# Optimization experiments

Hardware: AMD Instinct MI355X
Metric: run time of the kernel (lower is better)

## Reference

```python
import jax, jax.numpy as jnp
import numpy as np
import math

B, N, D = 4, 1024, 512
L, H, DH = 6, 8, 64
FF_INNER = 4 * D
NUM_BUCKETS, MAX_DIST = 32, 128
SCALE = 16.0  # cosine_sim_scale
ROT_DIM = 32  # min(32, dim_head)


def layernorm(x, g, stable=False, eps=1e-5):
    if stable:
        x = x / jax.lax.stop_gradient(jnp.max(x, axis=-1, keepdims=True))
    mean = jnp.mean(x, axis=-1, keepdims=True)
    var = jnp.mean(jnp.square(x - mean), axis=-1, keepdims=True)  # unbiased=False
    return (x - mean) * jax.lax.rsqrt(var + eps) * g


def l2norm(x, eps=1e-12):
    return x / jnp.maximum(jnp.linalg.norm(x, axis=-1, keepdims=True), eps)


def rotary_freqs(n):
    inv_freq = 1.0 / (10000.0 ** (jnp.arange(0, ROT_DIM, 2, dtype=jnp.float32) / ROT_DIM))
    f = jnp.arange(n, dtype=jnp.float32)[:, None] * inv_freq[None, :]  # [n, ROT_DIM/2]
    return jnp.repeat(f, 2, axis=-1)  # [n, ROT_DIM], interleaved pairs


def apply_rotary(t, freqs):
    # rotate only first ROT_DIM dims (rotary_embedding_torch semantics)
    rot, passd = t[..., :ROT_DIM], t[..., ROT_DIM:]
    x = rot.reshape(*rot.shape[:-1], ROT_DIM // 2, 2)
    rotated = jnp.stack((-x[..., 1], x[..., 0]), axis=-1).reshape(rot.shape)
    rot = rot * jnp.cos(freqs) + rotated * jnp.sin(freqs)
    return jnp.concatenate([rot, passd], axis=-1)


def rel_pos_bias(emb, i, j):
    # T5-style causal relative position buckets
    rel = jnp.arange(j)[None, :] - jnp.arange(i)[:, None]
    n = jnp.maximum(-rel, 0)
    max_exact = NUM_BUCKETS // 2
    val_large = max_exact + (
        jnp.log(jnp.maximum(n, 1).astype(jnp.float32) / max_exact)
        / math.log(MAX_DIST / max_exact) * (NUM_BUCKETS - max_exact)
    ).astype(jnp.int32)
    val_large = jnp.minimum(val_large, NUM_BUCKETS - 1)
    bucket = jnp.where(n < max_exact, n, val_large)
    return emb[bucket].transpose(2, 0, 1)  # [h, i, j]


def setup_inputs() -> dict:
    key = jax.random.key(0)
    ks = jax.random.split(key, 9)
    s = 0.02
    return {
        "x": jax.random.normal(ks[0], (B, N, D), jnp.float32),
        "rel_pos_emb": jax.random.normal(ks[1], (NUM_BUCKETS, H), jnp.float32) * s,
        "g_attn": jnp.ones((L, D), jnp.float32),
        "null_kv": jax.random.normal(ks[2], (L, 2, DH), jnp.float32),
        "Wq": jax.random.normal(ks[3], (L, D, H * DH), jnp.float32) * s,
        "Wkv": jax.random.normal(ks[4], (L, D, 2 * DH), jnp.float32) * s,
        "Wo": jax.random.normal(ks[5], (L, H * DH, D), jnp.float32) * s,
        "g_attn_out": jnp.ones((L, D), jnp.float32),
        "g_ff": jnp.ones((L, D), jnp.float32),
        "W1": jax.random.normal(ks[6], (L, D, 2 * FF_INNER), jnp.float32) * s,
        "W2": jax.random.normal(ks[7], (L, FF_INNER, D), jnp.float32) * s,
        "g_final": jnp.ones((D,), jnp.float32),
        "W_proj": jax.random.normal(ks[8], (D, D), jnp.float32) * s,
    }


def reference(x, rel_pos_emb, g_attn, null_kv, Wq, Wkv, Wo, g_attn_out, g_ff, W1, W2, g_final, W_proj):
    b, n, d = x.shape
    freqs = rotary_freqs(n)
    bias = rel_pos_bias(rel_pos_emb, n, n + 1)          # [h, n, n+1] (null kv column at j=0)
    causal = jnp.triu(jnp.ones((n, n + 1), dtype=bool), k=2)  # .triu(j - i + 1)
    neg = -jnp.finfo(x.dtype).max
    for l in range(L):
        # --- attention block ---
        xn = layernorm(x, g_attn[l])
        q = (xn @ Wq[l]).reshape(b, n, H, DH).transpose(0, 2, 1, 3) * SCALE  # b h n d
        k, v = jnp.split(xn @ Wkv[l], 2, axis=-1)                            # b n d (single-head kv)
        q = apply_rotary(q, freqs)
        k = apply_rotary(k, freqs)
        k = jnp.concatenate([jnp.broadcast_to(null_kv[l, 0], (b, 1, DH)), k], axis=1)
        v = jnp.concatenate([jnp.broadcast_to(null_kv[l, 1], (b, 1, DH)), v], axis=1)
        qn = l2norm(q) * math.sqrt(SCALE)   # cosine-sim attention
        kn = l2norm(k) * math.sqrt(SCALE)
        sim = jnp.einsum('bhid,bjd->bhij', qn, kn) + bias
        sim = jnp.where(causal, neg, sim)
        attn = jax.nn.softmax(sim.astype(jnp.float32), axis=-1).astype(x.dtype)
        o = jnp.einsum('bhij,bjd->bhid', attn, v).transpose(0, 2, 1, 3).reshape(b, n, H * DH)
        x = x + layernorm(o @ Wo[l], g_attn_out[l])
        # --- SwiGLU feedforward block ---
        hn = layernorm(x, g_ff[l])
        a, gate = jnp.split(hn @ W1[l], 2, axis=-1)
        x = x + (a * jax.nn.silu(gate)) @ W2[l]
    out = layernorm(x, g_final, stable=True)
    return out @ W_proj
```

## Files before the change

### kernel.cpp

```cpp
#include <hip/hip_runtime.h>
#include <hip/hip_bf16.h>
#include <cmath>

using bf16 = __hip_bfloat16;
typedef __bf16 v8bf __attribute__((ext_vector_type(8)));
typedef __bf16 v4bf __attribute__((ext_vector_type(4)));
typedef float  v4f  __attribute__((ext_vector_type(4)));

__device__ __forceinline__ float bf2f(bf16 x) { return __bfloat162float(x); }
__device__ __forceinline__ bf16  f2bf(float x) { return __float2bfloat16(x); }
__device__ __forceinline__ __bf16 tobf(float x) {
    bf16 h = __float2bfloat16(x);
    return __builtin_bit_cast(__bf16, h);
}

__device__ __forceinline__ void gll16(const bf16* g, bf16* l) {
    __builtin_amdgcn_global_load_lds(
        (const __attribute__((address_space(1))) unsigned int*)g,
        (__attribute__((address_space(3))) unsigned int*)l, 16, 0, 0);
}

__device__ __forceinline__ float ldin(const void* p, size_t i, int isf32) {
    if (isf32) return ((const float*)p)[i];
    return bf2f(((const bf16*)p)[i]);
}

__device__ __forceinline__ void ld8(const void* p, size_t base, int f, float v[8]) {
    if (f) {
        const float* pf = (const float*)p + base;
        float4 a = *(const float4*)pf, b = *(const float4*)(pf + 4);
        v[0]=a.x; v[1]=a.y; v[2]=a.z; v[3]=a.w;
        v[4]=b.x; v[5]=b.y; v[6]=b.z; v[7]=b.w;
    } else {
        v8bf a = *(const v8bf*)((const bf16*)p + base);
#pragma unroll
        for (int j = 0; j < 8; ++j) v[j] = (float)a[j];
    }
}

__device__ __forceinline__ float wave_sum(float v) {
#pragma unroll
    for (int o = 32; o > 0; o >>= 1) v += __shfl_xor(v, o, 64);
    return v;
}
__device__ __forceinline__ float wave_max(float v) {
#pragma unroll
    for (int o = 32; o > 0; o >>= 1) v = fmaxf(v, __shfl_xor(v, o, 64));
    return v;
}

__global__ void detect_k(const unsigned short* __restrict__ x, int* __restrict__ flag)
{
    __shared__ int s;
    int t = threadIdx.x;
    if (t == 0) s = 0;
    __syncthreads();
    int bad = 0;
    for (int i = t; i < 4096; i += 256) {
        int e = (x[i] >> 7) & 0xFF;
        if (e >= 147) bad++;
    }
    atomicAdd(&s, bad);
    __syncthreads();
    if (t == 0) *flag = (s > 64) ? 1 : 0;
}

__global__ __launch_bounds__(256)
void gemm_bt_silu(const bf16* __restrict__ A, const bf16* __restrict__ BT,
                  bf16* __restrict__ U, int K, int lda)
{
    __shared__ bf16 As[128 * 32];
    __shared__ bf16 Bs[128 * 32];
    const int t = threadIdx.x;
    const int lane = t & 63;
    const int wave = t >> 6;
    const int wm = (wave >> 1) * 64;
    const int wn = (wave & 1) * 64;
    const int bm = blockIdx.x * 128;
    const int bn = blockIdx.y * 128;
    const int fr = lane & 15;
    const int fk = (lane >> 4) * 8;

    v4f acc[4][4];
#pragma unroll
    for (int i = 0; i < 4; ++i)
#pragma unroll
        for (int j = 0; j < 4; ++j) { v4f z = {0.f, 0.f, 0.f, 0.f}; acc[i][j] = z; }

    for (int k0 = 0; k0 < K; k0 += 32) {
#pragma unroll
        for (int r = 0; r < 2; ++r) {
            int c = t + 256 * r;
            int row = c >> 2;
            int koff = (c & 3) * 8;
            gll16(A + (size_t)(bm + row) * lda + k0 + koff, &As[c * 8]);
            gll16(BT + (size_t)(bn + row) * K + k0 + koff, &Bs[c * 8]);
        }
        __syncthreads();
        v8bf af[4], bfr[4];
#pragma unroll
        for (int mt = 0; mt < 4; ++mt)
            af[mt] = *(const v8bf*)(&As[(wm + mt * 16 + fr) * 32 + fk]);
#pragma unroll
        for (int nt = 0; nt < 4; ++nt)
            bfr[nt] = *(const v8bf*)(&Bs[(wn + nt * 16 + fr) * 32 + fk]);
#pragma unroll
        for (int mt = 0; mt < 4; ++mt)
#pragma unroll
            for (int nt = 0; nt < 4; ++nt)
                acc[mt][nt] = __builtin_amdgcn_mfma_f32_16x16x32_bf16(
                    af[mt], bfr[nt], acc[mt][nt], 0, 0, 0);
        __syncthreads();
    }
    const int r0 = (lane >> 4) * 4;
    const int gbase = ((bn + wn) >> 6) * 32;
#pragma unroll
    for (int mt = 0; mt < 4; ++mt)
#pragma unroll
        for (int nt = 0; nt < 2; ++nt)
#pragma unroll
            for (int r = 0; r < 4; ++r) {
                int row = bm + wm + mt * 16 + r0 + r;
                int col = gbase + nt * 16 + fr;
                float a  = acc[mt][nt][r];
                float gg = acc[mt][nt + 2][r];
                U[(size_t)row * 2048 + col] = f2bf(a * (gg / (1.f + __expf(-gg))));
            }
}

__global__ __launch_bounds__(256)
void gemm64(const bf16* __restrict__ A, const bf16* __restrict__ BT,
            bf16* __restrict__ C, int M, int N, int K, int lda)
{
    __shared__ bf16 As[64 * 32];
    __shared__ bf16 Bs[128 * 32];
    const int t = threadIdx.x;
    const int lane = t & 63;
    const int wave = t >> 6;
    const int wm = (wave >> 1) * 32;
    const int wn = (wave & 1) * 64;
    const int bm = blockIdx.x * 64;
    const int bn = blockIdx.y * 128;
    const int fr = lane & 15;
    const int fk = (lane >> 4) * 8;

    v4f acc[2][4];
#pragma unroll
    for (int i = 0; i < 2; ++i)
#pragma unroll
        for (int j = 0; j < 4; ++j) { v4f z = {0.f, 0.f, 0.f, 0.f}; acc[i][j] = z; }

    for (int k0 = 0; k0 < K; k0 += 32) {
        {
            int row = t >> 2, koff = (t & 3) * 8;
            gll16(A + (size_t)(bm + row) * lda + k0 + koff, &As[t * 8]);
        }
#pragma unroll
        for (int r = 0; r < 2; ++r) {
            int c = t + 256 * r;
            int row = c >> 2, koff = (c & 3) * 8;
            gll16(BT + (size_t)(bn + row) * K + k0 + koff, &Bs[c * 8]);
        }
        __syncthreads();
        v8bf af[2], bfr[4];
#pragma unroll
        for (int mt = 0; mt < 2; ++mt)
            af[mt] = *(const v8bf*)(&As[(wm + mt * 16 + fr) * 32 + fk]);
#pragma unroll
        for (int nt = 0; nt < 4; ++nt)
            bfr[nt] = *(const v8bf*)(&Bs[(wn + nt * 16 + fr) * 32 + fk]);
#pragma unroll
        for (int mt = 0; mt < 2; ++mt)
#pragma unroll
            for (int nt = 0; nt < 4; ++nt)
                acc[mt][nt] = __builtin_amdgcn_mfma_f32_16x16x32_bf16(
                    af[mt], bfr[nt], acc[mt][nt], 0, 0, 0);
        __syncthreads();
    }
    const int r0 = (lane >> 4) * 4;
#pragma unroll
    for (int mt = 0; mt < 2; ++mt)
#pragma unroll
        for (int nt = 0; nt < 4; ++nt)
#pragma unroll
            for (int r = 0; r < 4; ++r) {
                int row = bm + wm + mt * 16 + r0 + r;
                int col = bn + wn + nt * 16 + fr;
                C[(size_t)row * N + col] = f2bf(acc[mt][nt][r]);
            }
}

__global__ __launch_bounds__(256)
void gemm64_out(const bf16* __restrict__ A, const bf16* __restrict__ BT,
                void* __restrict__ C, int M, int N, int K, int lda,
                const int* __restrict__ flag)
{
    __shared__ bf16 As[64 * 32];
    __shared__ bf16 Bs[128 * 32];
    const int f = *flag;
    const int t = threadIdx.x;
    const int lane = t & 63;
    const int wave = t >> 6;
    const int wm = (wave >> 1) * 32;
    const int wn = (wave & 1) * 64;
    const int bm = blockIdx.x * 64;
    const int bn = blockIdx.y * 128;
    const int fr = lane & 15;
    const int fk = (lane >> 4) * 8;

    v4f acc[2][4];
#pragma unroll
    for (int i = 0; i < 2; ++i)
#pragma unroll
        for (int j = 0; j < 4; ++j) { v4f z = {0.f, 0.f, 0.f, 0.f}; acc[i][j] = z; }

    for (int k0 = 0; k0 < K; k0 += 32) {
        {
            int row = t >> 2, koff = (t & 3) * 8;
            gll16(A + (size_t)(bm + row) * lda + k0 + koff, &As[t * 8]);
        }
#pragma unroll
        for (int r = 0; r < 2; ++r) {
            int c = t + 256 * r;
            int row = c >> 2, koff = (c & 3) * 8;
            gll16(BT + (size_t)(bn + row) * K + k0 + koff, &Bs[c * 8]);
        }
        __syncthreads();
        v8bf af[2], bfr[4];
#pragma unroll
        for (int mt = 0; mt < 2; ++mt)
            af[mt] = *(const v8bf*)(&As[(wm + mt * 16 + fr) * 32 + fk]);
#pragma unroll
        for (int nt = 0; nt < 4; ++nt)
            bfr[nt] = *(const v8bf*)(&Bs[(wn + nt * 16 + fr) * 32 + fk]);
#pragma unroll
        for (int mt = 0; mt < 2; ++mt)
#pragma unroll
            for (int nt = 0; nt < 4; ++nt)
                acc[mt][nt] = __builtin_amdgcn_mfma_f32_16x16x32_bf16(
                    af[mt], bfr[nt], acc[mt][nt], 0, 0, 0);
        __syncthreads();
    }
    const int r0 = (lane >> 4) * 4;
#pragma unroll
    for (int mt = 0; mt < 2; ++mt)
#pragma unroll
        for (int nt = 0; nt < 4; ++nt)
#pragma unroll
            for (int r = 0; r < 4; ++r) {
                int row = bm + wm + mt * 16 + r0 + r;
                int col = bn + wn + nt * 16 + fr;
                if (f) ((float*)C)[(size_t)row * N + col] = acc[mt][nt][r];
                else   ((bf16*)C)[(size_t)row * N + col] = f2bf(acc[mt][nt][r]);
            }
}

__global__ __launch_bounds__(256)
void transpose2_k(const void* __restrict__ in, bf16* __restrict__ out, int R, int C,
                  size_t inZ, size_t outZ, const int* __restrict__ flag)
{
    __shared__ bf16 tile[32][33];
    int f = *flag;
    size_t ioff = (size_t)blockIdx.z * inZ;
    bf16* dst = out + (size_t)blockIdx.z * outZ;
    int c0 = blockIdx.x * 32, r0 = blockIdx.y * 32;
    int tx = threadIdx.x, ty = threadIdx.y;
#pragma unroll
    for (int i = 0; i < 32; i += 8)
        tile[ty + i][tx] = f2bf(ldin(in, ioff + (size_t)(r0 + ty + i) * C + c0 + tx, f));
    __syncthreads();
#pragma unroll
    for (int i = 0; i < 32; i += 8)
        dst[(size_t)(c0 + ty + i) * R + r0 + tx] = tile[tx][ty + i];
}

__global__ __launch_bounds__(256)
void transposeW1_k(const void* __restrict__ in, bf16* __restrict__ out,
                   const int* __restrict__ flag)
{
    __shared__ bf16 tile[32][33];
    int f = *flag;
    size_t ioff = (size_t)blockIdx.z * (512ull * 4096);
    bf16* dst = out + (size_t)blockIdx.z * (512ull * 4096);
    int c0 = blockIdx.x * 32, r0 = blockIdx.y * 32;
    int tx = threadIdx.x, ty = threadIdx.y;
#pragma unroll
    for (int i = 0; i < 32; i += 8)
        tile[ty + i][tx] = f2bf(ldin(in, ioff + (size_t)(r0 + ty + i) * 4096 + c0 + tx, f));
    __syncthreads();
#pragma unroll
    for (int i = 0; i < 32; i += 8) {
        int j = c0 + ty + i;
        int jp = (j < 2048) ? (((j >> 5) << 6) | (j & 31))
                            : ((((j - 2048) >> 5) << 6) | 32 | (j & 31));
        dst[(size_t)jp * 512 + r0 + tx] = tile[tx][ty + i];
    }
}

__global__ __launch_bounds__(256)
void xinit_ln_k(const void* __restrict__ in, const void* __restrict__ g,
                const int* __restrict__ flag, float* __restrict__ x, bf16* __restrict__ xn)
{
    int f = *flag;
    int row = blockIdx.x * 4 + (threadIdx.x >> 6);
    int lane = threadIdx.x & 63;
    int c0 = lane * 8;
    float v[8];
    ld8(in, (size_t)row * 512 + c0, f, v);
    float* xr = x + (size_t)row * 512 + c0;
    *(float4*)xr       = make_float4(v[0], v[1], v[2], v[3]);
    *(float4*)(xr + 4) = make_float4(v[4], v[5], v[6], v[7]);
    float s = 0.f;
#pragma unroll
    for (int j = 0; j < 8; ++j) s += v[j];
    float mean = wave_sum(s) * (1.f / 512.f);
    float q = 0.f;
#pragma unroll
    for (int j = 0; j < 8; ++j) { float d = v[j] - mean; q += d * d; }
    float var = wave_sum(q) * (1.f / 512.f);
    float rstd = rsqrtf(var + 1e-5f);
    float gv[8];
    ld8(g, c0, f, gv);
    v8bf o;
#pragma unroll
    for (int j = 0; j < 8; ++j) o[j] = tobf((v[j] - mean) * rstd * gv[j]);
    *(v8bf*)(xn + (size_t)row * 512 + c0) = o;
}

__global__ __launch_bounds__(256)
void addln_ln_k(const bf16* __restrict__ tin, const void* __restrict__ g1, int g1off,
                const void* __restrict__ g2, int g2off, const int* __restrict__ flag,
                float* __restrict__ x, bf16* __restrict__ xn)
{
    int f = *flag;
    int row = blockIdx.x * 4 + (threadIdx.x >> 6);
    int lane = threadIdx.x & 63;
    int c0 = lane * 8;
    float tv[8];
    {
        v8bf a = *(const v8bf*)(tin + (size_t)row * 512 + c0);
#pragma unroll
        for (int j = 0; j < 8; ++j) tv[j] = (float)a[j];
    }
    float s = 0.f;
#pragma unroll
    for (int j = 0; j < 8; ++j) s += tv[j];
    float mean = wave_sum(s) * (1.f / 512.f);
    float q = 0.f;
#pragma unroll
    for (int j = 0; j < 8; ++j) { float d = tv[j] - mean; q += d * d; }
    float var = wave_sum(q) * (1.f / 512.f);
    float rstd = rsqrtf(var + 1e-5f);
    float g1v[8];
    ld8(g1, (size_t)g1off + c0, f, g1v);
    float* xr = x + (size_t)row * 512 + c0;
    float4 xa = *(float4*)xr, xb = *(float4*)(xr + 4);
    float nx[8] = {xa.x, xa.y, xa.z, xa.w, xb.x, xb.y, xb.z, xb.w};
#pragma unroll
    for (int j = 0; j < 8; ++j) nx[j] += (tv[j] - mean) * rstd * g1v[j];
    *(float4*)xr       = make_float4(nx[0], nx[1], nx[2], nx[3]);
    *(float4*)(xr + 4) = make_float4(nx[4], nx[5], nx[6], nx[7]);
    float s2 = 0.f;
#pragma unroll
    for (int j = 0; j < 8; ++j) s2 += nx[j];
    float mean2 = wave_sum(s2) * (1.f / 512.f);
    float q2 = 0.f;
#pragma unroll
    for (int j = 0; j < 8; ++j) { float e = nx[j] - mean2; q2 += e * e; }
    float var2 = wave_sum(q2) * (1.f / 512.f);
    float rstd2 = rsqrtf(var2 + 1e-5f);
    float g2v[8];
    ld8(g2, (size_t)g2off + c0, f, g2v);
    v8bf o;
#pragma unroll
    for (int j = 0; j < 8; ++j) o[j] = tobf((nx[j] - mean2) * rstd2 * g2v[j]);
    *(v8bf*)(xn + (size_t)row * 512 + c0) = o;
}

__global__ __launch_bounds__(256)
void add_ln_k(const bf16* __restrict__ tin, const void* __restrict__ g, int goff,
              const int* __restrict__ flag, int stable,
              float* __restrict__ x, bf16* __restrict__ xn)
{
    int f = *flag;
    int row = blockIdx.x * 4 + (threadIdx.x >> 6);
    int lane = threadIdx.x & 63;
    int c0 = lane * 8;
    float nx[8];
    {
        v8bf a = *(const v8bf*)(tin + (size_t)row * 512 + c0);
        float* xr = x + (size_t)row * 512 + c0;
        float4 xa = *(float4*)xr, xb = *(float4*)(xr + 4);
        float xv[8] = {xa.x, xa.y, xa.z, xa.w, xb.x, xb.y, xb.z, xb.w};
#pragma unroll
        for (int j = 0; j < 8; ++j) nx[j] = xv[j] + (float)a[j];
        *(float4*)xr       = make_float4(nx[0], nx[1], nx[2], nx[3]);
        *(float4*)(xr + 4) = make_float4(nx[4], nx[5], nx[6], nx[7]);
    }
    float v[8];
#pragma unroll
    for (int j = 0; j < 8; ++j) v[j] = nx[j];
    if (stable) {
        float m = v[0];
#pragma unroll
        for (int j = 1; j < 8; ++j) m = fmaxf(m, v[j]);
        float mx = wave_max(m);
#pragma unroll
        for (int j = 0; j < 8; ++j) v[j] /= mx;
    }
    float s = 0.f;
#pragma unroll
    for (int j = 0; j < 8; ++j) s += v[j];
    float mean = wave_sum(s) * (1.f / 512.f);
    float q = 0.f;
#pragma unroll
    for (int j = 0; j < 8; ++j) { float d = v[j] - mean; q += d * d; }
    float var = wave_sum(q) * (1.f / 512.f);
    float rstd = rsqrtf(var + 1e-5f);
    float gv[8];
    ld8(g, (size_t)goff + c0, f, gv);
    v8bf o;
#pragma unroll
    for (int j = 0; j < 8; ++j) o[j] = tobf((v[j] - mean) * rstd * gv[j]);
    *(v8bf*)(xn + (size_t)row * 512 + c0) = o;
}

__global__ __launch_bounds__(256)
void rotab_k(float2* __restrict__ tab)
{
    int idx = blockIdx.x * 256 + threadIdx.x;
    if (idx >= 16384) return;
    int n = idx >> 4, p = idx & 15;
    float ang = (float)n * expf((float)p * -0.5756462732f);
    tab[idx] = make_float2(cosf(ang), sinf(ang));
}

__global__ __launch_bounds__(256)
void bias_k(const void* __restrict__ rpe, const int* __restrict__ flag, float* __restrict__ tab)
{
    int f = *flag;
    int idx = blockIdx.x * 256 + threadIdx.x;
    if (idx >= 8 * 1025) return;
    int h = idx / 1025, dist = idx % 1025;
    int bkt;
    if (dist < 16) bkt = dist;
    else {
        bkt = 16 + (int)(logf((float)dist / 16.f) / logf(8.f) * 16.f);
        if (bkt > 31) bkt = 31;
    }
    tab[idx] = ldin(rpe, bkt * 8 + h, f) - 16.f;
}

__global__ __launch_bounds__(256)
void qkvprep_k(const bf16* __restrict__ qkv, const void* __restrict__ nkv, int nkoff,
               const int* __restrict__ flag, const float2* __restrict__ rtab,
               bf16* __restrict__ Q, bf16* __restrict__ K, bf16* __restrict__ Vt)
{
    int t = threadIdx.x, lane = t & 63;
    int bid = blockIdx.x;
    if (bid < 2048) {
        int rid = bid * 16 + (t >> 4);
        int h = rid & 7;
        int n = (rid >> 3) & 1023;
        int b = rid >> 13;
        int g16 = t & 15;
        int d0 = g16 * 4;
        v4bf a = *(const v4bf*)(qkv + (size_t)((b << 10) | n) * 640 + h * 64 + d0);
        float v[4];
#pragma unroll
        for (int j = 0; j < 4; ++j) v[j] = (float)a[j] * 16.f;
        if (d0 < 32) {
            float4 cs = *(const float4*)((const float*)rtab + (size_t)n * 32 + (size_t)(d0 >> 1) * 2);
            float r0 = v[0] * cs.x - v[1] * cs.y;
            float r1 = v[1] * cs.x + v[0] * cs.y;
            float r2 = v[2] * cs.z - v[3] * cs.w;
            float r3 = v[3] * cs.z + v[2] * cs.w;
            v[0] = r0; v[1] = r1; v[2] = r2; v[3] = r3;
        }
        float ss = v[0]*v[0] + v[1]*v[1] + v[2]*v[2] + v[3]*v[3];
#pragma unroll
        for (int o = 1; o < 16; o <<= 1) ss += __shfl_xor(ss, o, 64);
        float sc = 4.f / fmaxf(sqrtf(ss), 1e-12f);
        v4bf ov;
#pragma unroll
        for (int j = 0; j < 4; ++j) ov[j] = tobf(v[j] * sc);
        *(v4bf*)(Q + (((size_t)(b * 8 + h)) * 1024 + n) * 64 + d0) = ov;
    } else {
        int f = *flag;
        int rid = (bid - 2048) * 4 + (t >> 6);
        if (rid >= 4 * 1088) return;
        int j = rid % 1088;
        int b = rid / 1088;
        if (j >= 1025) {
            K[((size_t)b * 1088 + j) * 64 + lane] = f2bf(0.f);
            Vt[((size_t)b * 64 + lane) * 1088 + j] = f2bf(0.f);
            return;
        }
        float kv, vv;
        if (j == 0) {
            kv = ldin(nkv, nkoff + lane, f);
            vv = ldin(nkv, nkoff + 64 + lane, f);
        } else {
            int n = j - 1;
            const bf16* src = qkv + (size_t)(b * 1024 + n) * 640 + 512;
            kv = bf2f(src[lane]);
            vv = bf2f(src[64 + lane]);
            if (lane < 32) {
                float2 cs = rtab[n * 16 + (lane >> 1)];
                float other = __shfl_xor(kv, 1, 64);
                float rot = (lane & 1) ? other : -other;
                kv = kv * cs.x + rot * cs.y;
            }
        }
        float nrm = sqrtf(wave_sum(kv * kv));
        kv = kv / fmaxf(nrm, 1e-12f) * 4.f;
        K[((size_t)b * 1088 + j) * 64 + lane] = f2bf(kv);
        Vt[((size_t)b * 64 + lane) * 1088 + j] = f2bf(vv);
    }
}

__global__ __launch_bounds__(256)
void attn_mfma(const bf16* __restrict__ Q, const bf16* __restrict__ Kg,
               const bf16* __restrict__ Vtg, const float* __restrict__ bias,
               bf16* __restrict__ Op, float* __restrict__ ml)
{
    __shared__ bf16 Ks[64][72];
    __shared__ bf16 Vts[64][72];
    __shared__ bf16 Ps[4][16][72];
    __shared__ float bs[1088];
    const int bh = blockIdx.x, b = bh >> 3, h = bh & 7;
    const int yy = (int)gridDim.y - 1 - (int)blockIdx.y;
    const int sp = blockIdx.z;
    const int i0 = yy * 64;
    const int t = threadIdx.x, lane = t & 63, w = t >> 6;
    const int col = lane & 15, quad = lane >> 4, fk = quad * 8;
    const float* bt = bias + h * 1025;
    const bf16* Kb = Kg + (size_t)b * 1088 * 64;
    const bf16* Vb = Vtg + (size_t)b * 64 * 1088;

    for (int idx = t; idx < i0 + 64; idx += 256) bs[idx] = bt[idx];

    v8bf qf[2];
    const bf16* qrow = Q + ((size_t)bh * 1024 + i0 + w * 16 + col) * 64;
    qf[0] = *(const v8bf*)(qrow + fk);
    qf[1] = *(const v8bf*)(qrow + 32 + fk);

    v4f oacc[4];
#pragma unroll
    for (int dt = 0; dt < 4; ++dt) { v4f z = {0.f,0.f,0.f,0.f}; oacc[dt] = z; }
    float lpart[4] = {0.f, 0.f, 0.f, 0.f};

    const int nch = yy + 2;
    const int rr0 = t >> 3, co0 = (t & 7) * 8;
    const int rr1 = (t + 256) >> 3, co1 = co0;

    v8bf kr[2], vr[2];
    if (sp < nch) {
        int j0 = sp * 64;
        kr[0] = *(const v8bf*)(Kb + (size_t)(j0 + rr0) * 64 + co0);
        vr[0] = *(const v8bf*)(Vb + (size_t)rr0 * 1088 + j0 + co0);
        kr[1] = *(const v8bf*)(Kb + (size_t)(j0 + rr1) * 64 + co1);
        vr[1] = *(const v8bf*)(Vb + (size_t)rr1 * 1088 + j0 + co1);
    }

    for (int ch = sp; ch < nch; ch += 4) {
        const int j0 = ch * 64;
        __syncthreads();
        *(v8bf*)(&Ks[rr0][co0])  = kr[0];
        *(v8bf*)(&Vts[rr0][co0]) = vr[0];
        *(v8bf*)(&Ks[rr1][co1])  = kr[1];
        *(v8bf*)(&Vts[rr1][co1]) = vr[1];
        const int more = (ch + 4 < nch);
        if (more) {
            int j0n = (ch + 4) * 64;
            kr[0] = *(const v8bf*)(Kb + (size_t)(j0n + rr0) * 64 + co0);
            vr[0] = *(const v8bf*)(Vb + (size_t)rr0 * 1088 + j0n + co0);
            kr[1] = *(const v8bf*)(Kb + (size_t)(j0n + rr1) * 64 + co1);
            vr[1] = *(const v8bf*)(Vb + (size_t)rr1 * 1088 + j0n + co1);
        }
        __syncthreads();

        v4f sreg[4];
#pragma unroll
        for (int nt = 0; nt < 4; ++nt) {
            v4f z = {0.f,0.f,0.f,0.f};
            v8bf kf0 = *(const v8bf*)(&Ks[nt * 16 + col][fk]);
            v8bf kf1 = *(const v8bf*)(&Ks[nt * 16 + col][32 + fk]);
            z = __builtin_amdgcn_mfma_f32_16x16x32_bf16(qf[0], kf0, z, 0, 0, 0);
            z = __builtin_amdgcn_mfma_f32_16x16x32_bf16(qf[1], kf1, z, 0, 0, 0);
            sreg[nt] = z;
        }

        if (ch < yy) {
#pragma unroll
            for (int reg = 0; reg < 4; ++reg) {
                int i = i0 + w * 16 + quad * 4 + reg;
                int dbase = i - j0 - col;
#pragma unroll
                for (int nt = 0; nt < 4; ++nt) {
                    float pp = __expf(sreg[nt][reg] + bs[dbase - nt * 16]);
                    lpart[reg] += pp;
                    Ps[w][quad * 4 + reg][nt * 16 + col] = f2bf(pp);
                }
            }
        } else {
#pragma unroll
            for (int reg = 0; reg < 4; ++reg) {
                int i = i0 + w * 16 + quad * 4 + reg;
#pragma unroll
                for (int nt = 0; nt < 4; ++nt) {
                    int j = j0 + nt * 16 + col;
                    float pp = 0.f;
                    if (j <= i + 1 && j < 1025) {
                        int dist = i - j; if (dist < 0) dist = 0;
                        pp = __expf(sreg[nt][reg] + bs[dist]);
                    }
                    lpart[reg] += pp;
                    Ps[w][quad * 4 + reg][nt * 16 + col] = f2bf(pp);
                }
            }
        }

        v8bf pf[2];
        pf[0] = *(const v8bf*)(&Ps[w][col][fk]);
        pf[1] = *(const v8bf*)(&Ps[w][col][32 + fk]);
#pragma unroll
        for (int dt = 0; dt < 4; ++dt) {
#pragma unroll
            for (int ks = 0; ks < 2; ++ks) {
                v8bf vf = *(const v8bf*)(&Vts[dt * 16 + col][ks * 32 + fk]);
                oacc[dt] = __builtin_amdgcn_mfma_f32_16x16x32_bf16(pf[ks], vf, oacc[dt], 0, 0, 0);
            }
        }
    }

#pragma unroll
    for (int reg = 0; reg < 4; ++reg) {
#pragma unroll
        for (int o = 1; o < 16; o <<= 1) lpart[reg] += __shfl_xor(lpart[reg], o, 64);
    }

#pragma unroll
    for (int reg = 0; reg < 4; ++reg) {
        int i = i0 + w * 16 + quad * 4 + reg;
        size_t rbase = ((size_t)(sp * 32 + bh) * 1024 + i);
#pragma unroll
        for (int dt = 0; dt < 4; ++dt)
            Op[rbase * 64 + dt * 16 + col] = f2bf(oacc[dt][reg]);
        if (col == 0) ml[rbase] = lpart[reg];
    }
}

__global__ __launch_bounds__(256)
void attn_comb(const bf16* __restrict__ Op, const float* __restrict__ ml,
               bf16* __restrict__ O)
{
    int tid = blockIdx.x * 256 + threadIdx.x;
    int r = tid >> 3;
    int d0 = (tid & 7) * 8;
    float l = ml[r] + ml[32768 + r] + ml[65536 + r] + ml[98304 + r];
    float inv = 1.f / l;
    v8bf p0 = *(const v8bf*)(Op + (size_t)r * 64 + d0);
    v8bf p1 = *(const v8bf*)(Op + ((size_t)32768 + r) * 64 + d0);
    v8bf p2 = *(const v8bf*)(Op + ((size_t)65536 + r) * 64 + d0);
    v8bf p3 = *(const v8bf*)(Op + ((size_t)98304 + r) * 64 + d0);
    v8bf o;
#pragma unroll
    for (int j = 0; j < 8; ++j)
        o[j] = tobf(((float)p0[j] + (float)p1[j] + (float)p2[j] + (float)p3[j]) * inv);
    int bh = r >> 10, i = r & 1023, b = bh >> 3, h = bh & 7;
    *(v8bf*)(O + ((size_t)(b * 1024 + i)) * 512 + h * 64 + d0) = o;
}

extern "C" void kernel_launch(void* const* d_in, const int* in_sizes, int n_in,
                              void* d_out, int out_size, void* d_ws, size_t ws_size,
                              hipStream_t stream)
{
    const void* x_in     = d_in[0];
    const void* rpe      = d_in[1];
    const void* g_attn   = d_in[2];
    const void* null_kv  = d_in[3];
    const void* Wq       = d_in[4];
    const void* Wkv      = d_in[5];
    const void* Wo       = d_in[6];
    const void* g_attn_o = d_in[7];
    const void* g_ff     = d_in[8];
    const void* W1       = d_in[9];
    const void* W2       = d_in[10];
    const void* g_final  = d_in[11];
    const void* W_proj   = d_in[12];

    char* wp = (char*)d_ws;
    auto alloc = [&](size_t bytes) {
        char* p = wp; wp += (bytes + 255) & ~(size_t)255; return p;
    };
    float* xf    = (float*)alloc(4096ull * 512 * 4);
    bf16*  xn    = (bf16*) alloc(4096ull * 512 * 2);
    bf16*  tb    = (bf16*) alloc(4096ull * 512 * 2);
    bf16*  ub    = (bf16*) alloc(4096ull * 4096 * 2);
    bf16*  Kb    = (bf16*) alloc(4ull * 1088 * 64 * 2);
    bf16*  Vtb   = (bf16*) alloc(4ull * 64 * 1088 * 2);
    float* btab  = (float*)alloc(8ull * 1025 * 4);
    float2* rtab = (float2*)alloc(16384ull * 8);
    int*   dfl   = (int*)  alloc(256);
    bf16*  WqkvT = (bf16*) alloc(6ull * 640 * 512 * 2);
    bf16*  WoT   = (bf16*) alloc(6ull * 512 * 512 * 2);
    bf16*  W1T   = (bf16*) alloc(6ull * 4096 * 512 * 2);
    bf16*  W2T   = (bf16*) alloc(6ull * 512 * 2048 * 2);
    bf16*  WpT   = (bf16*) alloc(512ull * 512 * 2);
    bf16*  qkvb  = ub;
    bf16*  Qb    = ub + 2621440;
    bf16*  ob    = ub + 4718592;
    bf16*  Opart = ub + 6815744;
    float* mlprt = (float*)(ub + 15204352);

    detect_k<<<1, 256, 0, stream>>>((const unsigned short*)x_in, dfl);
    transpose2_k<<<dim3(16, 16, 6),  dim3(32, 8), 0, stream>>>(Wq, WqkvT, 512, 512, 512ull*512, 640ull*512, dfl);
    transpose2_k<<<dim3(4, 16, 6),   dim3(32, 8), 0, stream>>>(Wkv, WqkvT + 512ull*512, 512, 128, 512ull*128, 640ull*512, dfl);
    transpose2_k<<<dim3(16, 16, 6),  dim3(32, 8), 0, stream>>>(Wo, WoT, 512, 512, 512ull*512, 512ull*512, dfl);
    transposeW1_k<<<dim3(128, 16, 6), dim3(32, 8), 0, stream>>>(W1, W1T, dfl);
    transpose2_k<<<dim3(16, 64, 6),  dim3(32, 8), 0, stream>>>(W2, W2T, 2048, 512, 2048ull*512, 2048ull*512, dfl);
    transpose2_k<<<dim3(16, 16, 1),  dim3(32, 8), 0, stream>>>(W_proj, WpT, 512, 512, 512ull*512, 512ull*512, dfl);
    bias_k<<<33, 256, 0, stream>>>(rpe, dfl, btab);
    rotab_k<<<64, 256, 0, stream>>>(rtab);
    xinit_ln_k<<<1024, 256, 0, stream>>>(x_in, g_attn, dfl, xf, xn);

    for (int l = 0; l < 6; ++l) {
        gemm64<<<dim3(64, 5), 256, 0, stream>>>(xn, WqkvT + (size_t)l * 640 * 512, qkvb, 4096, 640, 512, 512);
        qkvprep_k<<<3136, 256, 0, stream>>>(qkvb, null_kv, l * 128, dfl, rtab, Qb, Kb, Vtb);
        attn_mfma<<<dim3(32, 16, 4), 256, 0, stream>>>(Qb, Kb, Vtb, btab, Opart, mlprt);
        attn_comb<<<1024, 256, 0, stream>>>(Opart, mlprt, ob);
        gemm64<<<dim3(64, 4), 256, 0, stream>>>(ob, WoT + (size_t)l * 512 * 512, tb, 4096, 512, 512, 512);
        addln_ln_k<<<1024, 256, 0, stream>>>(tb, g_attn_o, l * 512, g_ff, l * 512, dfl, xf, xn);
        gemm_bt_silu<<<dim3(32, 32), 256, 0, stream>>>(xn, W1T + (size_t)l * 4096 * 512, ub, 512, 512);
        gemm64<<<dim3(64, 4), 256, 0, stream>>>(ub, W2T + (size_t)l * 512 * 2048, tb, 4096, 512, 2048, 2048);
        if (l < 5)
            add_ln_k<<<1024, 256, 0, stream>>>(tb, g_attn, (l + 1) * 512, dfl, 0, xf, xn);
        else
            add_ln_k<<<1024, 256, 0, stream>>>(tb, g_final, 0, dfl, 1, xf, xn);
    }
    gemm64_out<<<dim3(64, 4), 256, 0, stream>>>(xn, WpT, d_out, 4096, 512, 512, 512, dfl);
}
```

Before: 963.4 us.

## Swizzle GEMM LDS tiles and drop split-K attention combine pass

The three MFMA GEMM kernels now XOR-swizzle the 8-element k-chunk index by row when loading A/B tiles into LDS, and read them back with the matching swizzled offset. The goal is to remove LDS bank conflicts on the fragment reads. Separately, the attention kernel no longer splits the key range four ways. Each block now walks all key chunks itself, normalises by the row sum and writes the output directly, which removes the attn_comb kernel and its partial-buffer traffic. The trade-off is a quarter as many attention blocks, so parallelism is lower and each block does more serial work.

```diff
diff --git a/kernel.cpp b/kernel.cpp
--- a/kernel.cpp
+++ b/kernel.cpp
@@ -64,6 +64,7 @@
     __syncthreads();
     if (t == 0) *flag = (s > 64) ? 1 : 0;
 }
+
 
 __global__ __launch_bounds__(256)
 void gemm_bt_silu(const bf16* __restrict__ A, const bf16* __restrict__ BT,
@@ -79,7 +80,7 @@
     const int bm = blockIdx.x * 128;
     const int bn = blockIdx.y * 128;
     const int fr = lane & 15;
-    const int fk = (lane >> 4) * 8;
+    const int fk = (((lane >> 4) ^ ((fr >> 1) & 3))) * 8;
 
     v4f acc[4][4];
 #pragma unroll
@@ -92,7 +93,7 @@
         for (int r = 0; r < 2; ++r) {
             int c = t + 256 * r;
             int row = c >> 2;
-            int koff = (c & 3) * 8;
+            int koff = ((c & 3) ^ ((row >> 1) & 3)) * 8;
             gll16(A + (size_t)(bm + row) * lda + k0 + koff, &As[c * 8]);
             gll16(BT + (size_t)(bn + row) * K + k0 + koff, &Bs[c * 8]);
         }
@@ -142,7 +143,7 @@
     const int bm = blockIdx.x * 64;
     const int bn = blockIdx.y * 128;
     const int fr = lane & 15;
-    const int fk = (lane >> 4) * 8;
+    const int fk = (((lane >> 4) ^ ((fr >> 1) & 3))) * 8;
 
     v4f acc[2][4];
 #pragma unroll
@@ -152,13 +153,15 @@
 
     for (int k0 = 0; k0 < K; k0 += 32) {
         {
-            int row = t >> 2, koff = (t & 3) * 8;
+            int row = t >> 2;
+            int koff = ((t & 3) ^ ((row >> 1) & 3)) * 8;
             gll16(A + (size_t)(bm + row) * lda + k0 + koff, &As[t * 8]);
         }
 #pragma unroll
         for (int r = 0; r < 2; ++r) {
             int c = t + 256 * r;
-            int row = c >> 2, koff = (c & 3) * 8;
+            int row = c >> 2;
+            int koff = ((c & 3) ^ ((row >> 1) & 3)) * 8;
             gll16(BT + (size_t)(bn + row) * K + k0 + koff, &Bs[c * 8]);
         }
         __syncthreads();
@@ -206,7 +209,7 @@
     const int bm = blockIdx.x * 64;
     const int bn = blockIdx.y * 128;
     const int fr = lane & 15;
-    const int fk = (lane >> 4) * 8;
+    const int fk = (((lane >> 4) ^ ((fr >> 1) & 3))) * 8;
 
     v4f acc[2][4];
 #pragma unroll
@@ -216,13 +219,15 @@
 
     for (int k0 = 0; k0 < K; k0 += 32) {
         {
-            int row = t >> 2, koff = (t & 3) * 8;
+            int row = t >> 2;
+            int koff = ((t & 3) ^ ((row >> 1) & 3)) * 8;
             gll16(A + (size_t)(bm + row) * lda + k0 + koff, &As[t * 8]);
         }
 #pragma unroll
         for (int r = 0; r < 2; ++r) {
             int c = t + 256 * r;
-            int row = c >> 2, koff = (c & 3) * 8;
+            int row = c >> 2;
+            int koff = ((c & 3) ^ ((row >> 1) & 3)) * 8;
             gll16(BT + (size_t)(bn + row) * K + k0 + koff, &Bs[c * 8]);
         }
         __syncthreads();
@@ -522,7 +527,7 @@
 __global__ __launch_bounds__(256)
 void attn_mfma(const bf16* __restrict__ Q, const bf16* __restrict__ Kg,
                const bf16* __restrict__ Vtg, const float* __restrict__ bias,
-               bf16* __restrict__ Op, float* __restrict__ ml)
+               bf16* __restrict__ O)
 {
     __shared__ bf16 Ks[64][72];
     __shared__ bf16 Vts[64][72];
@@ -530,7 +535,6 @@
     __shared__ float bs[1088];
     const int bh = blockIdx.x, b = bh >> 3, h = bh & 7;
     const int yy = (int)gridDim.y - 1 - (int)blockIdx.y;
-    const int sp = blockIdx.z;
     const int i0 = yy * 64;
     const int t = threadIdx.x, lane = t & 63, w = t >> 6;
     const int col = lane & 15, quad = lane >> 4, fk = quad * 8;
@@ -555,24 +559,22 @@
     const int rr1 = (t + 256) >> 3, co1 = co0;
 
     v8bf kr[2], vr[2];
-    if (sp < nch) {
-        int j0 = sp * 64;
-        kr[0] = *(const v8bf*)(Kb + (size_t)(j0 + rr0) * 64 + co0);
-        vr[0] = *(const v8bf*)(Vb + (size_t)rr0 * 1088 + j0 + co0);
-        kr[1] = *(const v8bf*)(Kb + (size_t)(j0 + rr1) * 64 + co1);
-        vr[1] = *(const v8bf*)(Vb + (size_t)rr1 * 1088 + j0 + co1);
-    }
-
-    for (int ch = sp; ch < nch; ch += 4) {
+    {
+        kr[0] = *(const v8bf*)(Kb + (size_t)rr0 * 64 + co0);
+        vr[0] = *(const v8bf*)(Vb + (size_t)rr0 * 1088 + co0);
+        kr[1] = *(const v8bf*)(Kb + (size_t)rr1 * 64 + co1);
+        vr[1] = *(const v8bf*)(Vb + (size_t)rr1 * 1088 + co1);
+    }
+
+    for (int ch = 0; ch < nch; ++ch) {
         const int j0 = ch * 64;
         __syncthreads();
         *(v8bf*)(&Ks[rr0][co0])  = kr[0];
         *(v8bf*)(&Vts[rr0][co0]) = vr[0];
         *(v8bf*)(&Ks[rr1][co1])  = kr[1];
         *(v8bf*)(&Vts[rr1][co1]) = vr[1];
-        const int more = (ch + 4 < nch);
-        if (more) {
-            int j0n = (ch + 4) * 64;
+        if (ch + 1 < nch) {
+            int j0n = (ch + 1) * 64;
             kr[0] = *(const v8bf*)(Kb + (size_t)(j0n + rr0) * 64 + co0);
             vr[0] = *(const v8bf*)(Vb + (size_t)rr0 * 1088 + j0n + co0);
             kr[1] = *(const v8bf*)(Kb + (size_t)(j0n + rr1) * 64 + co1);
@@ -638,38 +640,13 @@
     for (int reg = 0; reg < 4; ++reg) {
 #pragma unroll
         for (int o = 1; o < 16; o <<= 1) lpart[reg] += __shfl_xor(lpart[reg], o, 64);
-    }
-
-#pragma unroll
-    for (int reg = 0; reg < 4; ++reg) {
+        float inv = 1.f / lpart[reg];
         int i = i0 + w * 16 + quad * 4 + reg;
-        size_t rbase = ((size_t)(sp * 32 + bh) * 1024 + i);
+        bf16* orow = O + ((size_t)(b * 1024 + i)) * 512 + h * 64;
 #pragma unroll
         for (int dt = 0; dt < 4; ++dt)
-            Op[rbase * 64 + dt * 16 + col] = f2bf(oacc[dt][reg]);
-        if (col == 0) ml[rbase] = lpart[reg];
-    }
-}
-
-__global__ __launch_bounds__(256)
-void attn_comb(const bf16* __restrict__ Op, const float* __restrict__ ml,
-               bf16* __restrict__ O)
-{
-    int tid = blockIdx.x * 256 + threadIdx.x;
-    int r = tid >> 3;
-    int d0 = (tid & 7) * 8;
-    float l = ml[r] + ml[32768 + r] + ml[65536 + r] + ml[98304 + r];
-    float inv = 1.f / l;
-    v8bf p0 = *(const v8bf*)(Op + (size_t)r * 64 + d0);
-    v8bf p1 = *(const v8bf*)(Op + ((size_t)32768 + r) * 64 + d0);
-    v8bf p2 = *(const v8bf*)(Op + ((size_t)65536 + r) * 64 + d0);
-    v8bf p3 = *(const v8bf*)(Op + ((size_t)98304 + r) * 64 + d0);
-    v8bf o;
-#pragma unroll
-    for (int j = 0; j < 8; ++j)
-        o[j] = tobf(((float)p0[j] + (float)p1[j] + (float)p2[j] + (float)p3[j]) * inv);
-    int bh = r >> 10, i = r & 1023, b = bh >> 3, h = bh & 7;
-    *(v8bf*)(O + ((size_t)(b * 1024 + i)) * 512 + h * 64 + d0) = o;
+            orow[dt * 16 + col] = f2bf(oacc[dt][reg] * inv);
+    }
 }
 
 extern "C" void kernel_launch(void* const* d_in, const int* in_sizes, int n_in,
@@ -711,8 +688,6 @@
     bf16*  qkvb  = ub;
     bf16*  Qb    = ub + 2621440;
     bf16*  ob    = ub + 4718592;
-    bf16*  Opart = ub + 6815744;
-    float* mlprt = (float*)(ub + 15204352);
 
     detect_k<<<1, 256, 0, stream>>>((const unsigned short*)x_in, dfl);
     transpose2_k<<<dim3(16, 16, 6),  dim3(32, 8), 0, stream>>>(Wq, WqkvT, 512, 512, 512ull*512, 640ull*512, dfl);
@@ -728,8 +703,7 @@
     for (int l = 0; l < 6; ++l) {
         gemm64<<<dim3(64, 5), 256, 0, stream>>>(xn, WqkvT + (size_t)l * 640 * 512, qkvb, 4096, 640, 512, 512);
         qkvprep_k<<<3136, 256, 0, stream>>>(qkvb, null_kv, l * 128, dfl, rtab, Qb, Kb, Vtb);
-        attn_mfma<<<dim3(32, 16, 4), 256, 0, stream>>>(Qb, Kb, Vtb, btab, Opart, mlprt);
-        attn_comb<<<1024, 256, 0, stream>>>(Opart, mlprt, ob);
+        attn_mfma<<<dim3(32, 16), 256, 0, stream>>>(Qb, Kb, Vtb, btab, ob);
         gemm64<<<dim3(64, 4), 256, 0, stream>>>(ob, WoT + (size_t)l * 512 * 512, tb, 4096, 512, 512, 512);
         addln_ln_k<<<1024, 256, 0, stream>>>(tb, g_attn_o, l * 512, g_ff, l * 512, dfl, xf, xn);
         gemm_bt_silu<<<dim3(32, 32), 256, 0, stream>>>(xn, W1T + (size_t)l * 4096 * 512, ub, 512, 512);
```

New measurement: 936.0 us. -2.8%, faster.
